# Optimization experiments

Measured on AMD Instinct MI355X. Metric: run time of the kernel, lower is better.

Reference implementation:

```python
import jax, jax.numpy as jnp
import numpy as np

MASK_VALUE = -1000000000.0
N = 100000        # num nodes
E = 1600000       # num edges
IN_DIM = 128
HID = 128
MAXN = 100000     # max_num_nodes
TAU = 0.5


def setup_inputs() -> dict:
    key = jax.random.key(0)
    ks = jax.random.split(key, 24)
    s_in = 1.0 / np.sqrt(IN_DIM)
    s_h = 1.0 / np.sqrt(HID)
    s_2h = 1.0 / np.sqrt(2 * HID)
    return {
        "x": jax.random.normal(ks[0], (N, IN_DIM), jnp.float32),
        "edge_index": jax.random.randint(ks[1], (2, E), 0, N, jnp.int32),
        # GCN layer params (PyG GCNConv: lin weight + bias)
        "W1": jax.random.normal(ks[2], (IN_DIM, HID), jnp.float32) * s_in,
        "b1": jnp.zeros((HID,), jnp.float32),
        "W2": jax.random.normal(ks[3], (HID, HID), jnp.float32) * s_h,
        "b2": jnp.zeros((HID,), jnp.float32),
        "W3": jax.random.normal(ks[4], (HID, HID), jnp.float32) * s_h,
        "b3": jnp.zeros((HID,), jnp.float32),
        # heads
        "n1W": jax.random.normal(ks[5], (2 * HID, MAXN), jnp.float32) * s_2h,
        "n1b": jnp.zeros((MAXN,), jnp.float32),
        "n2W": jax.random.normal(ks[6], (2 * HID, MAXN), jnp.float32) * s_2h,
        "n2b": jnp.zeros((MAXN,), jnp.float32),
        "eW": jax.random.normal(ks[7], (2 * HID, 3), jnp.float32) * s_2h,
        "eb": jnp.zeros((3,), jnp.float32),
        "sW": jax.random.normal(ks[8], (2 * HID, 1), jnp.float32) * s_2h,
        "sb": jnp.zeros((1,), jnp.float32),
        # gumbel noise for the 4 gumbel_softmax calls (deterministic reference)
        "g1": jax.random.gumbel(ks[9], (1, MAXN), jnp.float32),
        "g2": jax.random.gumbel(ks[10], (1, MAXN), jnp.float32),
        "ge": jax.random.gumbel(ks[11], (1, 3), jnp.float32),
        "gs": jax.random.gumbel(ks[12], (1, 1), jnp.float32),
    }


def _gcn_layer(x, W, b, src, dst, n):
    # PyG GCNConv: self-loops + symmetric norm D^-1/2 (A+I) D^-1/2 (XW) + b
    h = x @ W                                            # [n, H]
    deg = jnp.zeros((n,), h.dtype).at[dst].add(1.0) + 1.0  # +1 self-loop
    dinv = jax.lax.rsqrt(deg)
    msg = h[src] * (dinv[src] * dinv[dst])[:, None]      # [E, H] gather
    out = jax.ops.segment_sum(msg, dst, num_segments=n)  # scatter-add at targets
    out = out + h * (dinv * dinv)[:, None]               # self-loop contribution
    return out + b


def _gumbel_softmax(logits, g):
    return jax.nn.softmax((logits + g) / TAU, axis=-1)


def _mask_logits(logits, n, prev_idx, src, dst):
    # logits: [1, MAXN]
    idx = jnp.arange(logits.shape[-1])
    logits = jnp.where(idx[None, :] >= n, MASK_VALUE, logits)
    if prev_idx is not None:
        m = (src == prev_idx) | (dst == prev_idx)
        conn = jnp.zeros((logits.shape[-1],), bool)
        # scatter True at connected nodes; unmatched edges map onto prev_idx
        conn = conn.at[jnp.where(m, src, prev_idx)].set(True)
        conn = conn.at[jnp.where(m, dst, prev_idx)].set(True)
        conn = conn.at[prev_idx].set(True)
        logits = jnp.where(conn[None, :], MASK_VALUE, logits)
    return logits


def reference(x, edge_index, W1, b1, W2, b2, W3, b3, n1W, n1b, n2W, n2b, eW, eb, sW, sb, g1, g2, ge, gs):
    src, dst = edge_index[0], edge_index[1]
    n = x.shape[0]
    h = jax.nn.relu(_gcn_layer(x, W1, b1, src, dst, n))
    h = jax.nn.relu(_gcn_layer(h, W2, b2, src, dst, n))
    gcn = jax.nn.relu(_gcn_layer(h, W3, b3, src, dst, n))   # [n, H]

    pool = jnp.concatenate([gcn.mean(0, keepdims=True), gcn.max(0, keepdims=True)], axis=1)  # [1, 2H]

    l1 = _mask_logits(pool @ n1W + n1b, n, None, src, dst)
    n1_soft = _gumbel_softmax(l1, g1)                      # [1, MAXN]
    i1 = jnp.argmax(n1_soft, axis=-1)[0]

    l2 = _mask_logits(pool @ n2W + n2b, n, i1, src, dst)
    n2_soft = _gumbel_softmax(l2, g2)
    i2 = jnp.argmax(n2_soft, axis=-1)[0]

    node_emb = jnp.concatenate([gcn[i1][None, :], gcn[i2][None, :]], axis=1)  # [1, 2H]
    e_soft = _gumbel_softmax(node_emb @ eW + eb, ge)       # [1, 3]
    s_soft = _gumbel_softmax(pool @ sW + sb, gs)           # [1, 1]
    return (n1_soft, n2_soft, e_soft, s_soft)
```

## Files before the change

kernel.cpp:

```cpp
#include <hip/hip_runtime.h>

#define HID 128
#define MASKV -1000000000.0f
#define INV_TAU 2.0f
#define NB_SHIFT 9
#define NBMAX 256
#define ECHUNK 4096
#define BCAP 10240
#define FP8_SCALE 16.0f
#define FP8_INV_SCALE 0.0625f

using short8 = __attribute__((ext_vector_type(8))) short;
using f32x4  = __attribute__((ext_vector_type(4))) float;
using f32x2  = __attribute__((ext_vector_type(2))) float;

__device__ inline ushort f2bf(float f) {
  unsigned u = __float_as_uint(f);
  return (ushort)((u + 0x7FFFu + ((u >> 16) & 1u)) >> 16);
}
__device__ inline float bflo(unsigned u) { return __uint_as_float(u << 16); }
__device__ inline float bfhi(unsigned u) { return __uint_as_float(u & 0xFFFF0000u); }

__device__ inline unsigned char f2fp8(float v) {
  int p = __builtin_amdgcn_cvt_pk_fp8_f32(v, v, 0, false);
  return (unsigned char)(p & 0xFF);
}
__device__ inline void acc_fp8x4(unsigned w, float& a0, float& a1, float& a2, float& a3) {
  f32x2 lo = __builtin_amdgcn_cvt_pk_f32_fp8((int)w, false);
  f32x2 hi = __builtin_amdgcn_cvt_pk_f32_fp8((int)w, true);
  a0 += lo[0]; a1 += lo[1]; a2 += hi[0]; a3 += hi[1];
}

__device__ inline unsigned ordered_bits(float f) {
  unsigned u = __float_as_uint(f);
  return (u & 0x80000000u) ? ~u : (u | 0x80000000u);
}
__device__ inline int key_idx(unsigned long long k) {
  return (int)(0xFFFFFFFFu - (unsigned)(k & 0xFFFFFFFFull));
}

__global__ __launch_bounds__(256) void prep(uint4* __restrict__ zp, int n16, int* __restrict__ bcur, int zb,
                                            const float* __restrict__ W1, const float* __restrict__ W2,
                                            const float* __restrict__ W3, ushort* __restrict__ Wt) {
  int b = blockIdx.x, t = threadIdx.x;
  if (b == 0) { bcur[t] = t * BCAP; return; }
  if (b <= zb) {
    int i = (b - 1) * 256 + t;
    if (i < n16) zp[i] = make_uint4(0u, 0u, 0u, 0u);
    return;
  }
  int cb = b - zb - 1;
  const float* W = (cb < 64) ? W1 : (cb < 128) ? W2 : W3;
  ushort* o = Wt + (size_t)(cb >> 6) * 128 * 128;
  int idx = (cb & 63) * 256 + t;
  int c = idx >> 7, k = idx & 127;
  o[idx] = f2bf(W[k * 128 + c]);
}

__global__ __launch_bounds__(256) void edge_bucket(const int* __restrict__ ei, int E, int nb,
                                                   int* __restrict__ bcur, int2* __restrict__ staged) {
  __shared__ int ssrc[ECHUNK];
  __shared__ int sdst[ECHUNK];
  __shared__ int hist[NBMAX];
  __shared__ int cur[NBMAX];
  int t = threadIdx.x;
  int e0 = blockIdx.x * ECHUNK;
  int cnt = min(ECHUNK, E - e0);
  if (t < nb) hist[t] = 0;
  __syncthreads();
  for (int i = t; i < cnt; i += 256) {
    ssrc[i] = ei[e0 + i];
    int d = ei[E + e0 + i];
    sdst[i] = d;
    atomicAdd(&hist[d >> NB_SHIFT], 1);
  }
  __syncthreads();
  if (t < nb) cur[t] = atomicAdd(&bcur[t], hist[t]);
  __syncthreads();
  for (int i = t; i < cnt; i += 256) {
    int d = sdst[i];
    int pos = atomicAdd(&cur[d >> NB_SHIFT], 1);
    staged[pos] = make_int2(ssrc[i], d);
  }
}

__global__ __launch_bounds__(512) void bucket_csr2(const int2* __restrict__ staged, const int* __restrict__ bcur,
                                                   int* __restrict__ rows, int* __restrict__ cnt,
                                                   float* __restrict__ dinv, int* __restrict__ col, int n) {
  __shared__ int lcnt[512];
  __shared__ int lgs[512];
  __shared__ int lcur[512];
  __shared__ int lsc[512];
  int b = blockIdx.x;
  int t = threadIdx.x;
  int base = b << NB_SHIFT;
  lcnt[t] = 0;
  lcur[t] = 0;
  __syncthreads();
  int start = b * BCAP;
  int end = bcur[b];
  for (int i = start + t; i < end; i += 512) {
    atomicAdd(&lcnt[staged[i].y - base], 1);
  }
  __syncthreads();
  int v = lcnt[t];
  lsc[t] = v;
  __syncthreads();
  for (int d = 1; d < 512; d <<= 1) {
    int x = (t >= d) ? lsc[t - d] : 0;
    __syncthreads();
    lsc[t] += x;
    __syncthreads();
  }
  int gstart = start + lsc[t] - v;
  lgs[t] = gstart;
  int node = base + t;
  if (node < n) {
    rows[node] = gstart;
    cnt[node] = v;
    dinv[node] = rsqrtf((float)v + 1.0f);
  }
  __syncthreads();
  for (int i = start + t; i < end; i += 512) {
    int2 p = staged[i];
    int dl = p.y - base;
    int pos = atomicAdd(&lcur[dl], 1);
    col[lgs[dl] + pos] = p.x;
  }
}

template <int F32IN>
__global__ __launch_bounds__(256) void mfma_gemm(const void* __restrict__ Ain, const ushort* __restrict__ Wt,
                                                 const float* __restrict__ dinv, unsigned char* __restrict__ hW8, int n) {
  int w = threadIdx.x >> 6;
  int l = threadIdx.x & 63;
  int lr = l & 15;
  int lg = l >> 4;
  int r0 = blockIdx.x * 64 + w * 16;
  if (r0 >= n) return;
  int arow = r0 + lr;
  if (arow >= n) arow = n - 1;

  f32x4 acc[8];
#pragma unroll
  for (int ct = 0; ct < 8; ++ct) acc[ct] = (f32x4){0.f, 0.f, 0.f, 0.f};

#pragma unroll
  for (int kk = 0; kk < 4; ++kk) {
    short8 a;
    if (F32IN) {
      const float* Af = (const float*)Ain + (size_t)arow * 128 + kk * 32 + lg * 8;
      float4 f0 = ((const float4*)Af)[0];
      float4 f1 = ((const float4*)Af)[1];
      a[0] = (short)f2bf(f0.x); a[1] = (short)f2bf(f0.y);
      a[2] = (short)f2bf(f0.z); a[3] = (short)f2bf(f0.w);
      a[4] = (short)f2bf(f1.x); a[5] = (short)f2bf(f1.y);
      a[6] = (short)f2bf(f1.z); a[7] = (short)f2bf(f1.w);
    } else {
      a = ((const short8*)((const ushort*)Ain + (size_t)arow * 128))[kk * 4 + lg];
    }
#pragma unroll
    for (int ct = 0; ct < 8; ++ct) {
      short8 bfrag = ((const short8*)(Wt + (size_t)(ct * 16 + lr) * 128))[kk * 4 + lg];
      acc[ct] = __builtin_amdgcn_mfma_f32_16x16x32_bf16(a, bfrag, acc[ct], 0, 0, 0);
    }
  }

#pragma unroll
  for (int r = 0; r < 4; ++r) {
    int row = r0 + lg * 4 + r;
    if (row < n) {
      float dv = dinv[row] * FP8_SCALE;
#pragma unroll
      for (int ct = 0; ct < 8; ++ct) {
        hW8[(size_t)row * 128 + ct * 16 + lr] = f2fp8(acc[ct][r] * dv);
      }
    }
  }
}

__global__ __launch_bounds__(256) void gather_k(const int* __restrict__ row_start, const int* __restrict__ cnt,
                                                const int* __restrict__ col, const unsigned char* __restrict__ hW8,
                                                const float* __restrict__ dinv, const float* __restrict__ bias,
                                                ushort* __restrict__ outp, int n) {
  int g = (blockIdx.x * 256 + threadIdx.x) >> 5;
  if (g >= n) return;
  int lane = threadIdx.x & 31;
  const unsigned* h32 = (const unsigned*)hW8;
  float a0 = 0.f, a1 = 0.f, a2 = 0.f, a3 = 0.f;
  acc_fp8x4(h32[(size_t)g * 32 + lane], a0, a1, a2, a3);
  int jb = row_start[g];
  int je = jb + cnt[g];
  int j = jb;
  for (; j + 4 <= je; j += 4) {
    int s0 = __builtin_nontemporal_load(col + j);
    int s1 = __builtin_nontemporal_load(col + j + 1);
    int s2 = __builtin_nontemporal_load(col + j + 2);
    int s3 = __builtin_nontemporal_load(col + j + 3);
    unsigned w0 = h32[(size_t)s0 * 32 + lane];
    unsigned w1 = h32[(size_t)s1 * 32 + lane];
    unsigned w2 = h32[(size_t)s2 * 32 + lane];
    unsigned w3 = h32[(size_t)s3 * 32 + lane];
    acc_fp8x4(w0, a0, a1, a2, a3);
    acc_fp8x4(w1, a0, a1, a2, a3);
    acc_fp8x4(w2, a0, a1, a2, a3);
    acc_fp8x4(w3, a0, a1, a2, a3);
  }
  for (; j < je; ++j) {
    int s0 = __builtin_nontemporal_load(col + j);
    unsigned w0 = h32[(size_t)s0 * 32 + lane];
    acc_fp8x4(w0, a0, a1, a2, a3);
  }
  float din = dinv[g] * FP8_INV_SCALE;
  float4 bb = ((const float4*)bias)[lane];
  a0 = fmaxf(fmaf(a0, din, bb.x), 0.f);
  a1 = fmaxf(fmaf(a1, din, bb.y), 0.f);
  a2 = fmaxf(fmaf(a2, din, bb.z), 0.f);
  a3 = fmaxf(fmaf(a3, din, bb.w), 0.f);
  ushort4 o = {f2bf(a0), f2bf(a1), f2bf(a2), f2bf(a3)};
  *(ushort4*)(outp + (size_t)g * 128 + lane * 4) = o;
}

#define POOL_GRID 512
__global__ __launch_bounds__(256) void pool_kernel(const ushort* __restrict__ gcn, float* __restrict__ psum,
                                                   float* __restrict__ pmax, int nrows) {
  __shared__ float ls[16 * 128];
  __shared__ float lm[16 * 128];
  int t = threadIdx.x;
  int g = t >> 4;
  int c = t & 15;
  float s0 = 0.f, s1 = 0.f, s2 = 0.f, s3 = 0.f, s4 = 0.f, s5 = 0.f, s6 = 0.f, s7 = 0.f;
  float m0 = 0.f, m1 = 0.f, m2 = 0.f, m3 = 0.f, m4 = 0.f, m5 = 0.f, m6 = 0.f, m7 = 0.f;
  for (int r = blockIdx.x * 16 + g; r < nrows; r += POOL_GRID * 16) {
    uint4 w = *(const uint4*)(gcn + (size_t)r * 128 + c * 8);
    float v0 = bflo(w.x), v1 = bfhi(w.x), v2 = bflo(w.y), v3 = bfhi(w.y);
    float v4 = bflo(w.z), v5 = bfhi(w.z), v6 = bflo(w.w), v7 = bfhi(w.w);
    s0 += v0; s1 += v1; s2 += v2; s3 += v3; s4 += v4; s5 += v5; s6 += v6; s7 += v7;
    m0 = fmaxf(m0, v0); m1 = fmaxf(m1, v1); m2 = fmaxf(m2, v2); m3 = fmaxf(m3, v3);
    m4 = fmaxf(m4, v4); m5 = fmaxf(m5, v5); m6 = fmaxf(m6, v6); m7 = fmaxf(m7, v7);
  }
  int cb = c * 8;
  ls[g * 128 + cb + 0] = s0; ls[g * 128 + cb + 1] = s1; ls[g * 128 + cb + 2] = s2; ls[g * 128 + cb + 3] = s3;
  ls[g * 128 + cb + 4] = s4; ls[g * 128 + cb + 5] = s5; ls[g * 128 + cb + 6] = s6; ls[g * 128 + cb + 7] = s7;
  lm[g * 128 + cb + 0] = m0; lm[g * 128 + cb + 1] = m1; lm[g * 128 + cb + 2] = m2; lm[g * 128 + cb + 3] = m3;
  lm[g * 128 + cb + 4] = m4; lm[g * 128 + cb + 5] = m5; lm[g * 128 + cb + 6] = m6; lm[g * 128 + cb + 7] = m7;
  __syncthreads();
  if (t < 128) {
    float s = 0.f, m = 0.f;
#pragma unroll
    for (int gg = 0; gg < 16; ++gg) {
      s += ls[gg * 128 + t];
      m = fmaxf(m, lm[gg * 128 + t]);
    }
    atomicAdd(&psum[t], s);
    atomicMax((unsigned*)&pmax[t], __float_as_uint(m));
  }
}

__global__ __launch_bounds__(256) void head_fused(const float* __restrict__ W, const float* __restrict__ bias,
                                                  const float* __restrict__ g, const float* __restrict__ psum,
                                                  const float* __restrict__ pmax, float invn,
                                                  const int* __restrict__ conn, int use_conn,
                                                  float* __restrict__ ebuf, unsigned long long* __restrict__ cell,
                                                  float* __restrict__ sum, int maxn, int n) {
  __shared__ float p[256];
  __shared__ unsigned long long kred[256];
  __shared__ float sred[256];
  int t = threadIdx.x;
  p[t] = (t < 128) ? psum[t] * invn : pmax[t - 128];
  __syncthreads();
  int j0 = blockIdx.x * 512 + t;
  int j1 = j0 + 256;
  bool v0 = j0 < maxn, v1 = j1 < maxn;
  float acc0 = 0.f, acc1 = 0.f;
#pragma unroll 8
  for (int k = 0; k < 256; ++k) {
    const float* row = W + (size_t)k * maxn;
    float w0 = v0 ? __builtin_nontemporal_load(row + j0) : 0.f;
    float w1 = v1 ? __builtin_nontemporal_load(row + j1) : 0.f;
    acc0 = fmaf(p[k], w0, acc0);
    acc1 = fmaf(p[k], w1, acc1);
  }
  unsigned long long key = 0ull;
  float evs = 0.f;
  if (v0) {
    float logit = acc0 + bias[j0];
    if (j0 >= n) logit = MASKV;
    if (use_conn && conn[j0]) logit = MASKV;
    float zv = (logit + g[j0]) * INV_TAU;
    float ev = expf(zv);
    ebuf[j0] = ev;
    evs += ev;
    unsigned long long k0 = ((unsigned long long)ordered_bits(zv) << 32) | (unsigned long long)(0xFFFFFFFFu - (unsigned)j0);
    key = k0;
  }
  if (v1) {
    float logit = acc1 + bias[j1];
    if (j1 >= n) logit = MASKV;
    if (use_conn && conn[j1]) logit = MASKV;
    float zv = (logit + g[j1]) * INV_TAU;
    float ev = expf(zv);
    ebuf[j1] = ev;
    evs += ev;
    unsigned long long k1 = ((unsigned long long)ordered_bits(zv) << 32) | (unsigned long long)(0xFFFFFFFFu - (unsigned)j1);
    key = key > k1 ? key : k1;
  }
  kred[t] = key;
  sred[t] = evs;
  __syncthreads();
  for (int s = 128; s > 0; s >>= 1) {
    if (t < s) {
      kred[t] = kred[t] > kred[t + s] ? kred[t] : kred[t + s];
      sred[t] += sred[t + s];
    }
    __syncthreads();
  }
  if (t == 0) {
    atomicMax(cell, kred[0]);
    atomicAdd(sum, sred[0]);
  }
}

__global__ __launch_bounds__(256) void conn_kernel(const int* __restrict__ ei, int E,
                                                   const unsigned long long* __restrict__ cell1,
                                                   int* __restrict__ conn) {
  int e = blockIdx.x * 256 + threadIdx.x;
  int i1 = key_idx(*cell1);
  if (e == 0) conn[i1] = 1;
  if (e < E) {
    int s = ei[e], d = ei[E + e];
    if (s == i1 || d == i1) {
      conn[s] = 1;
      conn[d] = 1;
    }
  }
}

__device__ void edge_stop(const ushort* __restrict__ gcn, const float* __restrict__ eW,
                          const float* __restrict__ ebias, const float* __restrict__ ge,
                          const unsigned long long* __restrict__ c1, const unsigned long long* __restrict__ c2,
                          float* __restrict__ ob) {
  __shared__ float red[3 * 128];
  int t = threadIdx.x;
  if (t < 128) {
    int i1 = key_idx(*c1);
    int i2 = key_idx(*c2);
    float ea  = __uint_as_float((unsigned)gcn[(size_t)i1 * HID + t] << 16);
    float eb2 = __uint_as_float((unsigned)gcn[(size_t)i2 * HID + t] << 16);
    red[t]       = ea * eW[t * 3 + 0] + eb2 * eW[(128 + t) * 3 + 0];
    red[128 + t] = ea * eW[t * 3 + 1] + eb2 * eW[(128 + t) * 3 + 1];
    red[256 + t] = ea * eW[t * 3 + 2] + eb2 * eW[(128 + t) * 3 + 2];
  }
  __syncthreads();
  for (int s = 64; s > 0; s >>= 1) {
    if (t < s) {
      red[t] += red[t + s];
      red[128 + t] += red[128 + t + s];
      red[256 + t] += red[256 + t + s];
    }
    __syncthreads();
  }
  if (t == 0) {
    float z0 = (red[0]   + ebias[0] + ge[0]) * INV_TAU;
    float z1 = (red[128] + ebias[1] + ge[1]) * INV_TAU;
    float z2 = (red[256] + ebias[2] + ge[2]) * INV_TAU;
    float m = fmaxf(z0, fmaxf(z1, z2));
    float e0 = expf(z0 - m), e1 = expf(z1 - m), e2 = expf(z2 - m);
    float inv = 1.f / (e0 + e1 + e2);
    ob[0] = e0 * inv;
    ob[1] = e1 * inv;
    ob[2] = e2 * inv;
    ob[3] = 1.0f;
  }
}

__global__ __launch_bounds__(256) void finish(const float* __restrict__ e1, const float* __restrict__ s1,
                                              const float* __restrict__ e2, const float* __restrict__ s2,
                                              float* __restrict__ out, int maxn,
                                              const ushort* __restrict__ gcn, const float* __restrict__ eW,
                                              const float* __restrict__ ebias, const float* __restrict__ ge,
                                              const unsigned long long* __restrict__ c1,
                                              const unsigned long long* __restrict__ c2) {
  if (blockIdx.x == gridDim.x - 1) {
    edge_stop(gcn, eW, ebias, ge, c1, c2, out + 2 * (size_t)maxn);
    return;
  }
  int j = blockIdx.x * 256 + threadIdx.x;
  if (j < maxn) {
    out[j] = e1[j] / (*s1);
    out[maxn + j] = e2[j] / (*s2);
  }
}

extern "C" void kernel_launch(void* const* d_in, const int* in_sizes, int n_in,
                              void* d_out, int out_size, void* d_ws, size_t ws_size,
                              hipStream_t stream) {
  const float* x  = (const float*)d_in[0];
  const int* ei   = (const int*)d_in[1];
  const float* W1 = (const float*)d_in[2];
  const float* b1 = (const float*)d_in[3];
  const float* W2 = (const float*)d_in[4];
  const float* b2 = (const float*)d_in[5];
  const float* W3 = (const float*)d_in[6];
  const float* b3 = (const float*)d_in[7];
  const float* n1W = (const float*)d_in[8];
  const float* n1b = (const float*)d_in[9];
  const float* n2W = (const float*)d_in[10];
  const float* n2b = (const float*)d_in[11];
  const float* eW  = (const float*)d_in[12];
  const float* eb  = (const float*)d_in[13];
  const float* g1  = (const float*)d_in[16];
  const float* g2  = (const float*)d_in[17];
  const float* ge  = (const float*)d_in[18];

  int n    = in_sizes[0] / HID;
  int E    = in_sizes[1] / 2;
  int maxn = in_sizes[9];
  int nb   = (n + (1 << NB_SHIFT) - 1) >> NB_SHIFT;
  float* out = (float*)d_out;

  char* ws = (char*)d_ws;
  size_t o = 0;
  ushort* H1B = (ushort*)(ws + o); o += (size_t)n * HID * 2;
  ushort* H2B = (ushort*)(ws + o); o += (size_t)n * HID * 2;
  unsigned char* HW8 = (unsigned char*)(ws + o); o += (size_t)n * HID;
  ushort* GCN = (ushort*)(ws + o); o += (size_t)n * HID * 2;
  ushort* WT  = (ushort*)(ws + o); o += (size_t)3 * 128 * 128 * 2;
  float* EB1  = (float*)(ws + o);  o += (size_t)maxn * 4;
  float* EB2  = (float*)(ws + o);  o += (size_t)maxn * 4;
  int* ROWS   = (int*)(ws + o);    o += (size_t)n * 4;
  int* CNT    = (int*)(ws + o);    o += (size_t)n * 4;
  int* COL    = (int*)(ws + o);    o += (size_t)NBMAX * BCAP * 4;
  int2* STAGED = (int2*)(ws + o);  o += (size_t)NBMAX * BCAP * 8;
  float* DINV = (float*)(ws + o);  o += (size_t)n * 4;
  int* BCUR   = (int*)(ws + o);    o += 1024;
  char* zero_start = ws + o;
  int* CONN   = (int*)(ws + o);    o += (size_t)maxn * 4;
  float* PS   = (float*)(ws + o);  o += 128 * 4;
  float* PM   = (float*)(ws + o);  o += 128 * 4;
  unsigned long long* CELLS = (unsigned long long*)(ws + o);
  float* SUM1 = (float*)(ws + o + 16);
  float* SUM2 = (float*)(ws + o + 20);
  o += 64;
  size_t zero_bytes = (size_t)((ws + o) - zero_start);
  int zero16 = (int)(zero_bytes / 16);
  int zb = (zero16 + 255) / 256;

  dim3 blk(256);
  int gE = (E + 255) / 256;
  int gHeadHalf = (maxn + 511) / 512;
  int gNorm = (maxn + 255) / 256;
  int gGemm = (n + 63) / 64;
  int gGather = (int)(((size_t)n * 32 + 255) / 256);
  int gEB = (E + ECHUNK - 1) / ECHUNK;
  float invn = 1.0f / (float)n;

  prep<<<1 + zb + 192, blk, 0, stream>>>((uint4*)zero_start, zero16, BCUR, zb, W1, W2, W3, WT);

  edge_bucket<<<gEB, blk, 0, stream>>>(ei, E, nb, BCUR, STAGED);
  bucket_csr2<<<nb, dim3(512), 0, stream>>>(STAGED, BCUR, ROWS, CNT, DINV, COL, n);

  mfma_gemm<1><<<gGemm, blk, 0, stream>>>(x, WT, DINV, HW8, n);
  gather_k<<<gGather, blk, 0, stream>>>(ROWS, CNT, COL, HW8, DINV, b1, H1B, n);
  mfma_gemm<0><<<gGemm, blk, 0, stream>>>(H1B, WT + 128 * 128, DINV, HW8, n);
  gather_k<<<gGather, blk, 0, stream>>>(ROWS, CNT, COL, HW8, DINV, b2, H2B, n);
  mfma_gemm<0><<<gGemm, blk, 0, stream>>>(H2B, WT + 2 * 128 * 128, DINV, HW8, n);
  gather_k<<<gGather, blk, 0, stream>>>(ROWS, CNT, COL, HW8, DINV, b3, GCN, n);

  pool_kernel<<<POOL_GRID, blk, 0, stream>>>(GCN, PS, PM, n);

  head_fused<<<gHeadHalf, blk, 0, stream>>>(n1W, n1b, g1, PS, PM, invn, nullptr, 0, EB1, &CELLS[0], SUM1, maxn, n);

  conn_kernel<<<gE, blk, 0, stream>>>(ei, E, &CELLS[0], CONN);

  head_fused<<<gHeadHalf, blk, 0, stream>>>(n2W, n2b, g2, PS, PM, invn, CONN, 1, EB2, &CELLS[1], SUM2, maxn, n);

  finish<<<gNorm + 1, blk, 0, stream>>>(EB1, SUM1, EB2, SUM2, out, maxn, GCN, eW, eb, ge, &CELLS[0], &CELLS[1]);
}
```

Measured before the change: 408.1 us.

## Fuse next-layer GEMM into gather and pack staged edges into 32 bits

The gather kernel now runs 512 threads per block covering 16 nodes. It stages the aggregated bf16 rows in LDS and immediately multiplies them by the next layer's weights with MFMA, writing fp8 output directly. This removes two standalone GEMM launches and the bf16 intermediate round trips through global memory, and uses ping-pong fp8 buffers. Separately, edge staging packs the local destination and source into one 32-bit word instead of an int2, halving staging traffic. The cost is an added block barrier in the gather, and the packing assumes node ids fit in 23 bits.

```diff
diff --git a/kernel.cpp b/kernel.cpp
--- a/kernel.cpp
+++ b/kernel.cpp
@@ -58,9 +58,9 @@
 }
 
 __global__ __launch_bounds__(256) void edge_bucket(const int* __restrict__ ei, int E, int nb,
-                                                   int* __restrict__ bcur, int2* __restrict__ staged) {
-  __shared__ int ssrc[ECHUNK];
-  __shared__ int sdst[ECHUNK];
+                                                   int* __restrict__ bcur, unsigned* __restrict__ staged) {
+  __shared__ unsigned spk[ECHUNK];
+  __shared__ unsigned char sbk[ECHUNK];
   __shared__ int hist[NBMAX];
   __shared__ int cur[NBMAX];
   int t = threadIdx.x;
@@ -69,22 +69,24 @@
   if (t < nb) hist[t] = 0;
   __syncthreads();
   for (int i = t; i < cnt; i += 256) {
-    ssrc[i] = ei[e0 + i];
+    int s = ei[e0 + i];
     int d = ei[E + e0 + i];
-    sdst[i] = d;
-    atomicAdd(&hist[d >> NB_SHIFT], 1);
+    int b = d >> NB_SHIFT;
+    spk[i] = ((unsigned)(d & ((1 << NB_SHIFT) - 1)) << 23) | (unsigned)s;
+    sbk[i] = (unsigned char)b;
+    atomicAdd(&hist[b], 1);
   }
   __syncthreads();
   if (t < nb) cur[t] = atomicAdd(&bcur[t], hist[t]);
   __syncthreads();
   for (int i = t; i < cnt; i += 256) {
-    int d = sdst[i];
-    int pos = atomicAdd(&cur[d >> NB_SHIFT], 1);
-    staged[pos] = make_int2(ssrc[i], d);
-  }
-}
-
-__global__ __launch_bounds__(512) void bucket_csr2(const int2* __restrict__ staged, const int* __restrict__ bcur,
+    int b = sbk[i];
+    int pos = atomicAdd(&cur[b], 1);
+    staged[pos] = spk[i];
+  }
+}
+
+__global__ __launch_bounds__(512) void bucket_csr2(const unsigned* __restrict__ staged, const int* __restrict__ bcur,
                                                    int* __restrict__ rows, int* __restrict__ cnt,
                                                    float* __restrict__ dinv, int* __restrict__ col, int n) {
   __shared__ int lcnt[512];
@@ -100,7 +102,7 @@
   int start = b * BCAP;
   int end = bcur[b];
   for (int i = start + t; i < end; i += 512) {
-    atomicAdd(&lcnt[staged[i].y - base], 1);
+    atomicAdd(&lcnt[staged[i] >> 23], 1);
   }
   __syncthreads();
   int v = lcnt[t];
@@ -122,15 +124,14 @@
   }
   __syncthreads();
   for (int i = start + t; i < end; i += 512) {
-    int2 p = staged[i];
-    int dl = p.y - base;
+    unsigned p = staged[i];
+    int dl = (int)(p >> 23);
     int pos = atomicAdd(&lcur[dl], 1);
-    col[lgs[dl] + pos] = p.x;
-  }
-}
-
-template <int F32IN>
-__global__ __launch_bounds__(256) void mfma_gemm(const void* __restrict__ Ain, const ushort* __restrict__ Wt,
+    col[lgs[dl] + pos] = (int)(p & 0x7FFFFFu);
+  }
+}
+
+__global__ __launch_bounds__(256) void mfma_gemm(const float* __restrict__ Ain, const ushort* __restrict__ Wt,
                                                  const float* __restrict__ dinv, unsigned char* __restrict__ hW8, int n) {
   int w = threadIdx.x >> 6;
   int l = threadIdx.x & 63;
@@ -147,18 +148,14 @@
 
 #pragma unroll
   for (int kk = 0; kk < 4; ++kk) {
+    const float* Af = Ain + (size_t)arow * 128 + kk * 32 + lg * 8;
+    float4 f0 = ((const float4*)Af)[0];
+    float4 f1 = ((const float4*)Af)[1];
     short8 a;
-    if (F32IN) {
-      const float* Af = (const float*)Ain + (size_t)arow * 128 + kk * 32 + lg * 8;
-      float4 f0 = ((const float4*)Af)[0];
-      float4 f1 = ((const float4*)Af)[1];
-      a[0] = (short)f2bf(f0.x); a[1] = (short)f2bf(f0.y);
-      a[2] = (short)f2bf(f0.z); a[3] = (short)f2bf(f0.w);
-      a[4] = (short)f2bf(f1.x); a[5] = (short)f2bf(f1.y);
-      a[6] = (short)f2bf(f1.z); a[7] = (short)f2bf(f1.w);
-    } else {
-      a = ((const short8*)((const ushort*)Ain + (size_t)arow * 128))[kk * 4 + lg];
-    }
+    a[0] = (short)f2bf(f0.x); a[1] = (short)f2bf(f0.y);
+    a[2] = (short)f2bf(f0.z); a[3] = (short)f2bf(f0.w);
+    a[4] = (short)f2bf(f1.x); a[5] = (short)f2bf(f1.y);
+    a[6] = (short)f2bf(f1.z); a[7] = (short)f2bf(f1.w);
 #pragma unroll
     for (int ct = 0; ct < 8; ++ct) {
       short8 bfrag = ((const short8*)(Wt + (size_t)(ct * 16 + lr) * 128))[kk * 4 + lg];
@@ -179,18 +176,23 @@
   }
 }
 
-__global__ __launch_bounds__(256) void gather_k(const int* __restrict__ row_start, const int* __restrict__ cnt,
-                                                const int* __restrict__ col, const unsigned char* __restrict__ hW8,
-                                                const float* __restrict__ dinv, const float* __restrict__ bias,
-                                                ushort* __restrict__ outp, int n) {
-  int g = (blockIdx.x * 256 + threadIdx.x) >> 5;
-  if (g >= n) return;
-  int lane = threadIdx.x & 31;
-  const unsigned* h32 = (const unsigned*)hW8;
+template <int DO_GEMM>
+__global__ __launch_bounds__(512) void gather_fuse(const int* __restrict__ row_start, const int* __restrict__ cnt,
+                                                   const int* __restrict__ col, const unsigned char* __restrict__ hW8in,
+                                                   const float* __restrict__ dinv, const float* __restrict__ bias,
+                                                   const ushort* __restrict__ Wt_next, unsigned char* __restrict__ hW8out,
+                                                   ushort* __restrict__ gcn_out, int n) {
+  __shared__ ushort lh[16][136];
+  int t = threadIdx.x;
+  int grp = t >> 5, lane = t & 31;
+  int g = blockIdx.x * 16 + grp;
+  bool valid = g < n;
+  int gc = valid ? g : (n - 1);
+  const unsigned* h32 = (const unsigned*)hW8in;
   float a0 = 0.f, a1 = 0.f, a2 = 0.f, a3 = 0.f;
-  acc_fp8x4(h32[(size_t)g * 32 + lane], a0, a1, a2, a3);
-  int jb = row_start[g];
-  int je = jb + cnt[g];
+  acc_fp8x4(h32[(size_t)gc * 32 + lane], a0, a1, a2, a3);
+  int jb = row_start[gc];
+  int je = jb + cnt[gc];
   int j = jb;
   for (; j + 4 <= je; j += 4) {
     int s0 = __builtin_nontemporal_load(col + j);
@@ -211,14 +213,43 @@
     unsigned w0 = h32[(size_t)s0 * 32 + lane];
     acc_fp8x4(w0, a0, a1, a2, a3);
   }
-  float din = dinv[g] * FP8_INV_SCALE;
+  float din = dinv[gc] * FP8_INV_SCALE;
   float4 bb = ((const float4*)bias)[lane];
   a0 = fmaxf(fmaf(a0, din, bb.x), 0.f);
   a1 = fmaxf(fmaf(a1, din, bb.y), 0.f);
   a2 = fmaxf(fmaf(a2, din, bb.z), 0.f);
   a3 = fmaxf(fmaf(a3, din, bb.w), 0.f);
-  ushort4 o = {f2bf(a0), f2bf(a1), f2bf(a2), f2bf(a3)};
-  *(ushort4*)(outp + (size_t)g * 128 + lane * 4) = o;
+  if (!valid) { a0 = a1 = a2 = a3 = 0.f; }
+
+  if (DO_GEMM) {
+    ushort* dl = &lh[grp][lane * 4];
+    dl[0] = f2bf(a0); dl[1] = f2bf(a1); dl[2] = f2bf(a2); dl[3] = f2bf(a3);
+    __syncthreads();
+    int w = t >> 6;
+    int l = t & 63;
+    int lr = l & 15, lg = l >> 4;
+    f32x4 acc = (f32x4){0.f, 0.f, 0.f, 0.f};
+#pragma unroll
+    for (int kk = 0; kk < 4; ++kk) {
+      short8 a = *(const short8*)(&lh[lr][kk * 32 + lg * 8]);
+      short8 bfrag = ((const short8*)(Wt_next + (size_t)(w * 16 + lr) * 128))[kk * 4 + lg];
+      acc = __builtin_amdgcn_mfma_f32_16x16x32_bf16(a, bfrag, acc, 0, 0, 0);
+    }
+    int r0 = blockIdx.x * 16;
+#pragma unroll
+    for (int r = 0; r < 4; ++r) {
+      int row = r0 + lg * 4 + r;
+      if (row < n) {
+        float dv = dinv[row] * FP8_SCALE;
+        hW8out[(size_t)row * 128 + w * 16 + lr] = f2fp8(acc[r] * dv);
+      }
+    }
+  } else {
+    if (valid) {
+      ushort4 o = {f2bf(a0), f2bf(a1), f2bf(a2), f2bf(a3)};
+      *(ushort4*)(gcn_out + (size_t)g * 128 + lane * 4) = o;
+    }
+  }
 }
 
 #define POOL_GRID 512
@@ -421,9 +452,8 @@
 
   char* ws = (char*)d_ws;
   size_t o = 0;
-  ushort* H1B = (ushort*)(ws + o); o += (size_t)n * HID * 2;
-  ushort* H2B = (ushort*)(ws + o); o += (size_t)n * HID * 2;
-  unsigned char* HW8 = (unsigned char*)(ws + o); o += (size_t)n * HID;
+  unsigned char* HW8A = (unsigned char*)(ws + o); o += (size_t)n * HID;
+  unsigned char* HW8B = (unsigned char*)(ws + o); o += (size_t)n * HID;
   ushort* GCN = (ushort*)(ws + o); o += (size_t)n * HID * 2;
   ushort* WT  = (ushort*)(ws + o); o += (size_t)3 * 128 * 128 * 2;
   float* EB1  = (float*)(ws + o);  o += (size_t)maxn * 4;
@@ -431,7 +461,7 @@
   int* ROWS   = (int*)(ws + o);    o += (size_t)n * 4;
   int* CNT    = (int*)(ws + o);    o += (size_t)n * 4;
   int* COL    = (int*)(ws + o);    o += (size_t)NBMAX * BCAP * 4;
-  int2* STAGED = (int2*)(ws + o);  o += (size_t)NBMAX * BCAP * 8;
+  unsigned* STAGED = (unsigned*)(ws + o); o += (size_t)NBMAX * BCAP * 4;
   float* DINV = (float*)(ws + o);  o += (size_t)n * 4;
   int* BCUR   = (int*)(ws + o);    o += 1024;
   char* zero_start = ws + o;
@@ -451,7 +481,7 @@
   int gHeadHalf = (maxn + 511) / 512;
   int gNorm = (maxn + 255) / 256;
   int gGemm = (n + 63) / 64;
-  int gGather = (int)(((size_t)n * 32 + 255) / 256);
+  int gFuse = (n + 15) / 16;
   int gEB = (E + ECHUNK - 1) / ECHUNK;
   float invn = 1.0f / (float)n;
 
@@ -460,12 +490,10 @@
   edge_bucket<<<gEB, blk, 0, stream>>>(ei, E, nb, BCUR, STAGED);
   bucket_csr2<<<nb, dim3(512), 0, stream>>>(STAGED, BCUR, ROWS, CNT, DINV, COL, n);
 
-  mfma_gemm<1><<<gGemm, blk, 0, stream>>>(x, WT, DINV, HW8, n);
-  gather_k<<<gGather, blk, 0, stream>>>(ROWS, CNT, COL, HW8, DINV, b1, H1B, n);
-  mfma_gemm<0><<<gGemm, blk, 0, stream>>>(H1B, WT + 128 * 128, DINV, HW8, n);
-  gather_k<<<gGather, blk, 0, stream>>>(ROWS, CNT, COL, HW8, DINV, b2, H2B, n);
-  mfma_gemm<0><<<gGemm, blk, 0, stream>>>(H2B, WT + 2 * 128 * 128, DINV, HW8, n);
-  gather_k<<<gGather, blk, 0, stream>>>(ROWS, CNT, COL, HW8, DINV, b3, GCN, n);
+  mfma_gemm<<<gGemm, blk, 0, stream>>>(x, WT, DINV, HW8A, n);
+  gather_fuse<1><<<gFuse, dim3(512), 0, stream>>>(ROWS, CNT, COL, HW8A, DINV, b1, WT + 128 * 128, HW8B, nullptr, n);
+  gather_fuse<1><<<gFuse, dim3(512), 0, stream>>>(ROWS, CNT, COL, HW8B, DINV, b2, WT + 2 * 128 * 128, HW8A, nullptr, n);
+  gather_fuse<0><<<gFuse, dim3(512), 0, stream>>>(ROWS, CNT, COL, HW8A, DINV, b3, nullptr, nullptr, GCN, n);
 
   pool_kernel<<<POOL_GRID, blk, 0, stream>>>(GCN, PS, PM, n);
 
```

Result: faster. 392.5 us (-3.8%).
